# Performance work log

Hardware: AMD Instinct MI355X
Metric: run time of the kernel (lower is better)

Reference implementation:

```python
import jax, jax.numpy as jnp
import numpy as np

B, D, T = 32, 256, 2048
Z_NUM, Z_DIM = 1024, 256


def setup_inputs() -> dict:
    key = jax.random.key(0)
    k1, k2 = jax.random.split(key)
    z = jax.random.normal(k1, (B, D, T), dtype=jnp.float32)
    embedding = jax.random.normal(k2, (Z_NUM, Z_DIM), dtype=jnp.float32)
    return {"z": z, "embedding": embedding}


def reference(z, embedding):
    # z: [B, D, T] (time_last=True), embedding: [z_num, z_dim]
    Bv, Dv, Tv = z.shape
    sg = jax.lax.stop_gradient
    # flatten to [N, D] with N = B*T
    zf = jnp.transpose(z, (0, 2, 1)).reshape(-1, Dv)
    # squared-euclidean distances [N, z_num]
    distances = (jnp.sum(zf * zf, axis=1, keepdims=True)
                 + jnp.sum(embedding * embedding, axis=1)
                 - 2.0 * (zf @ embedding.T))
    encoding_idx = jnp.argmin(distances, axis=1)          # [N]
    z_vq = embedding[encoding_idx]                        # [N, D] codebook gather
    # perplexity via scatter-add histogram (equiv. to one-hot scatter + column sum)
    counts = jnp.zeros((embedding.shape[0],), zf.dtype).at[encoding_idx].add(1.0)
    avg_probs = counts / zf.shape[0]
    perplexity = jnp.exp(-jnp.sum(avg_probs * jnp.log(avg_probs + 1e-10)))
    # commitment / codebook losses (reduction='mean', normalize=False)
    z_qut_loss = jnp.mean((z_vq - sg(zf)) ** 2)
    z_enc_loss = jnp.mean((sg(z_vq) - zf) ** 2)
    # straight-through estimator
    z_vq_st = zf + sg(z_vq - zf)
    out = jnp.transpose(z_vq_st.reshape(Bv, Tv, Dv), (0, 2, 1))  # back to [B, D, T]
    return out, z_qut_loss, z_enc_loss, perplexity
```

## Files before the change

### kernel.cpp

```cpp
#include <hip/hip_runtime.h>


typedef _Float16 f16;
typedef _Float16 f16x8 __attribute__((ext_vector_type(8)));
typedef float f32x4 __attribute__((ext_vector_type(4)));

#define NROWS 65536
#define THRESH 0.02f
#define AMB_CAP 32768

#define MERGE_T2(v1, i1, v2, i2, ov1, oi1, ov2, oi2)                      \
  do {                                                                    \
    if (ov1 < v1 || (ov1 == v1 && oi1 < i1)) {                            \
      if (v1 < ov2 || (v1 == ov2 && i1 < oi2)) { v2 = v1; i2 = i1; }      \
      else { v2 = ov2; i2 = oi2; }                                        \
      v1 = ov1; i1 = oi1;                                                 \
    } else if (ov1 < v2 || (ov1 == v2 && oi1 < i2)) { v2 = ov1; i2 = oi1; } \
  } while (0)

__global__ void k0_prep(const float* __restrict__ emb, f16* __restrict__ eh,
                        f16* __restrict__ el, float* __restrict__ enorm,
                        float* __restrict__ counts, float* __restrict__ loss,
                        int* __restrict__ ambc) {
  int c = blockIdx.x, d = threadIdx.x;
  float v = emb[c * 256 + d];
  f16 h = (f16)v;
  f16 l = (f16)(v - (float)h);
  eh[c * 256 + d] = h;
  el[c * 256 + d] = l;
  float s = v * v;
#pragma unroll
  for (int o = 32; o; o >>= 1) s += __shfl_down(s, o, 64);
  __shared__ float red[4];
  if ((d & 63) == 0) red[d >> 6] = s;
  __syncthreads();
  if (d == 0) enorm[c] = red[0] + red[1] + red[2] + red[3];
  if (c == 0) {
    for (int i = d; i < 1024; i += 256) counts[i] = 0.f;
    if (d == 0) { *loss = 0.f; *ambc = 0; }
  }
}

__global__ void kp_split(const float* __restrict__ z, f16* __restrict__ zh,
                         f16* __restrict__ zl) {
  __shared__ float F[64][65];
  int bid = blockIdx.x;
  int b = bid >> 7;
  int rem = bid & 127;
  int t0 = (rem >> 2) << 6;
  int dd0 = (rem & 3) << 6;
  int tid = threadIdx.x;
  int tl = tid & 63, dr = tid >> 6;
  const float* zp = z + ((size_t)b * 256 + dd0 + dr) * 2048 + t0 + tl;
#pragma unroll
  for (int i = 0; i < 16; ++i)
    F[dr + i * 4][tl] = zp[(size_t)i * 4 * 2048];
  __syncthreads();
  int r = tid >> 2, q = tid & 3;
  f16x8 h0, h1, l0, l1;
#pragma unroll
  for (int j = 0; j < 8; ++j) {
    float v = F[q * 16 + j][r];
    f16 h = (f16)v; h0[j] = h; l0[j] = (f16)(v - (float)h);
  }
#pragma unroll
  for (int j = 0; j < 8; ++j) {
    float v = F[q * 16 + 8 + j][r];
    f16 h = (f16)v; h1[j] = h; l1[j] = (f16)(v - (float)h);
  }
  size_t n = (size_t)b * 2048 + t0 + r;
  f16* ph = zh + n * 256 + dd0 + q * 16;
  f16* pl = zl + n * 256 + dd0 + q * 16;
  *(f16x8*)(ph) = h0; *(f16x8*)(ph + 8) = h1;
  *(f16x8*)(pl) = l0; *(f16x8*)(pl + 8) = l1;
}

__device__ __forceinline__ void k1_epilogue(
    f32x4 (&acc)[4][4], const float* en_s, float* rv1, int* ri1, float* rv2, int* ri2,
    int tid, int wr, int wc, int g, int r16, int rowTile, int chunk, int cBase,
    float* cv1, int* ci1, float* cv2, int* ci2) {
  float en[4];
#pragma unroll
  for (int ni = 0; ni < 4; ++ni) en[ni] = en_s[wc * 64 + ni * 16 + r16];
#pragma unroll
  for (int mi = 0; mi < 4; ++mi) {
#pragma unroll
    for (int r = 0; r < 4; ++r) {
      float v1 = 1e38f, v2 = 1e38f; int i1 = 0x7fffffff, i2 = 0x7fffffff;
#pragma unroll
      for (int ni = 0; ni < 4; ++ni) {
        float v = en[ni] - 2.0f * acc[mi][ni][r];
        int idx = cBase + wc * 64 + ni * 16 + r16;
        if (v < v1 || (v == v1 && idx < i1)) { v2 = v1; i2 = i1; v1 = v; i1 = idx; }
        else if (v < v2 || (v == v2 && idx < i2)) { v2 = v; i2 = idx; }
      }
#pragma unroll
      for (int o = 1; o < 16; o <<= 1) {
        float ov1 = __shfl_xor(v1, o, 64); int oi1 = __shfl_xor(i1, o, 64);
        float ov2 = __shfl_xor(v2, o, 64); int oi2 = __shfl_xor(i2, o, 64);
        MERGE_T2(v1, i1, v2, i2, ov1, oi1, ov2, oi2);
      }
      if (r16 == 0) {
        int row = wr * 64 + mi * 16 + g * 4 + r;
        rv1[row * 2 + wc] = v1; ri1[row * 2 + wc] = i1;
        rv2[row * 2 + wc] = v2; ri2[row * 2 + wc] = i2;
      }
    }
  }
  __syncthreads();
  if (tid < 128) {
    float v1 = rv1[tid * 2], ov1 = rv1[tid * 2 + 1];
    int   i1 = ri1[tid * 2], oi1 = ri1[tid * 2 + 1];
    float v2 = rv2[tid * 2], ov2 = rv2[tid * 2 + 1];
    int   i2 = ri2[tid * 2], oi2 = ri2[tid * 2 + 1];
    MERGE_T2(v1, i1, v2, i2, ov1, oi1, ov2, oi2);
    size_t n = (size_t)rowTile * 128 + tid;
    cv1[(size_t)chunk * NROWS + n] = v1;
    ci1[(size_t)chunk * NROWS + n] = i1;
    cv2[(size_t)chunk * NROWS + n] = v2;
    ci2[(size_t)chunk * NROWS + n] = i2;
  }
}

__launch_bounds__(256, 2)
__global__ void k1p_argmin(const f16* __restrict__ zh, const f16* __restrict__ zl,
                           const f16* __restrict__ eh, const f16* __restrict__ el,
                           const float* __restrict__ enorm,
                           float* __restrict__ cv1, int* __restrict__ ci1,
                           float* __restrict__ cv2, int* __restrict__ ci2) {
  __shared__ f16x8 Ah[128 * 5], Al[128 * 5], Bh[128 * 5], Bl[128 * 5];
  __shared__ float en_s[128];
  __shared__ float rv1[256], rv2[256];
  __shared__ int ri1[256], ri2[256];

  int bid = blockIdx.x;
  int x = bid & 7, j = bid >> 3;
  int rowTile = x * 64 + (j >> 3);
  int chunk = j & 7;
  int n0 = rowTile * 128;
  int cBase = chunk << 7;

  int tid = threadIdx.x;
  int lane = tid & 63;
  int wid = tid >> 6;
  int wr = wid >> 1, wc = wid & 1;
  int g = lane >> 4, r16 = lane & 15;

  if (tid < 128) en_s[tid] = enorm[cBase + tid];

  f32x4 acc[4][4] = {};

  int tt = tid & 127;
  int kk2 = tid >> 7;
  const f16* zhb = zh + ((size_t)(n0 + tt)) * 256 + kk2 * 16;
  const f16* zlb = zl + ((size_t)(n0 + tt)) * 256 + kk2 * 16;
  const f16* ehb = eh + ((size_t)(cBase + tt)) * 256 + kk2 * 16;
  const f16* elb = el + ((size_t)(cBase + tt)) * 256 + kk2 * 16;
  int s0 = tt * 5 + kk2 * 2, s1 = s0 + 1;

  for (int ks = 0; ks < 8; ++ks) {
    if (ks) __syncthreads();
    Ah[s0] = *(const f16x8*)(zhb + ks * 32);
    Ah[s1] = *(const f16x8*)(zhb + ks * 32 + 8);
    Al[s0] = *(const f16x8*)(zlb + ks * 32);
    Al[s1] = *(const f16x8*)(zlb + ks * 32 + 8);
    Bh[s0] = *(const f16x8*)(ehb + ks * 32);
    Bh[s1] = *(const f16x8*)(ehb + ks * 32 + 8);
    Bl[s0] = *(const f16x8*)(elb + ks * 32);
    Bl[s1] = *(const f16x8*)(elb + ks * 32 + 8);
    __syncthreads();
    f16x8 ah[4], al[4], bh[4], bl[4];
#pragma unroll
    for (int mi = 0; mi < 4; ++mi) {
      int row = wr * 64 + mi * 16 + r16;
      ah[mi] = Ah[row * 5 + g];
      al[mi] = Al[row * 5 + g];
    }
#pragma unroll
    for (int ni = 0; ni < 4; ++ni) {
      int code = wc * 64 + ni * 16 + r16;
      bh[ni] = Bh[code * 5 + g];
      bl[ni] = Bl[code * 5 + g];
    }
#pragma unroll
    for (int mi = 0; mi < 4; ++mi)
#pragma unroll
      for (int ni = 0; ni < 4; ++ni) {
        acc[mi][ni] = __builtin_amdgcn_mfma_f32_16x16x32_f16(ah[mi], bh[ni], acc[mi][ni], 0, 0, 0);
        acc[mi][ni] = __builtin_amdgcn_mfma_f32_16x16x32_f16(ah[mi], bl[ni], acc[mi][ni], 0, 0, 0);
        acc[mi][ni] = __builtin_amdgcn_mfma_f32_16x16x32_f16(al[mi], bh[ni], acc[mi][ni], 0, 0, 0);
      }
  }
  k1_epilogue(acc, en_s, rv1, ri1, rv2, ri2, tid, wr, wc, g, r16, rowTile, chunk,
              cBase, cv1, ci1, cv2, ci2);
}

__launch_bounds__(256, 2)
__global__ void k1_argmin(const float* __restrict__ z, const f16* __restrict__ eh,
                          const f16* __restrict__ el, const float* __restrict__ enorm,
                          float* __restrict__ cv1, int* __restrict__ ci1,
                          float* __restrict__ cv2, int* __restrict__ ci2) {
  __shared__ f16x8 Ah[128 * 5], Al[128 * 5], Bh[128 * 5], Bl[128 * 5];
  __shared__ float en_s[128];
  __shared__ float rv1[256], rv2[256];
  __shared__ int ri1[256], ri2[256];

  int bid = blockIdx.x;
  int x = bid & 7, j = bid >> 3;
  int rowTile = x * 64 + (j >> 3);
  int chunk = j & 7;
  int bb = rowTile >> 4;
  int t0 = (rowTile & 15) << 7;
  int cBase = chunk << 7;

  int tid = threadIdx.x;
  int lane = tid & 63;
  int wid = tid >> 6;
  int wr = wid >> 1, wc = wid & 1;
  int g = lane >> 4, r16 = lane & 15;

  if (tid < 128) en_s[tid] = enorm[cBase + tid];

  f32x4 acc[4][4] = {};

  int tt = tid & 127;
  int kk2 = tid >> 7;
  const float* zbase = z + ((size_t)bb * 256 + kk2 * 16) * 2048 + t0 + tt;
  const f16* ehbase = eh + ((size_t)(cBase + tt)) * 256 + kk2 * 16;
  const f16* elbase = el + ((size_t)(cBase + tt)) * 256 + kk2 * 16;
  int s0 = tt * 5 + kk2 * 2, s1 = s0 + 1;

  for (int ks = 0; ks < 8; ++ks) {
    if (ks) __syncthreads();
    {
      const float* zp = zbase + (size_t)ks * 32 * 2048;
      f16x8 h8, l8;
#pragma unroll
      for (int cj = 0; cj < 8; ++cj) {
        float v = zp[cj * 2048];
        f16 h = (f16)v; h8[cj] = h; l8[cj] = (f16)(v - (float)h);
      }
      Ah[s0] = h8; Al[s0] = l8;
#pragma unroll
      for (int cj = 0; cj < 8; ++cj) {
        float v = zp[(8 + cj) * 2048];
        f16 h = (f16)v; h8[cj] = h; l8[cj] = (f16)(v - (float)h);
      }
      Ah[s1] = h8; Al[s1] = l8;
    }
    {
      const f16* ep = ehbase + ks * 32;
      Bh[s0] = *(const f16x8*)(ep);
      Bh[s1] = *(const f16x8*)(ep + 8);
      const f16* ep2 = elbase + ks * 32;
      Bl[s0] = *(const f16x8*)(ep2);
      Bl[s1] = *(const f16x8*)(ep2 + 8);
    }
    __syncthreads();
    f16x8 ah[4], al[4], bh[4], bl[4];
#pragma unroll
    for (int mi = 0; mi < 4; ++mi) {
      int row = wr * 64 + mi * 16 + r16;
      ah[mi] = Ah[row * 5 + g];
      al[mi] = Al[row * 5 + g];
    }
#pragma unroll
    for (int ni = 0; ni < 4; ++ni) {
      int code = wc * 64 + ni * 16 + r16;
      bh[ni] = Bh[code * 5 + g];
      bl[ni] = Bl[code * 5 + g];
    }
#pragma unroll
    for (int mi = 0; mi < 4; ++mi)
#pragma unroll
      for (int ni = 0; ni < 4; ++ni) {
        acc[mi][ni] = __builtin_amdgcn_mfma_f32_16x16x32_f16(ah[mi], bh[ni], acc[mi][ni], 0, 0, 0);
        acc[mi][ni] = __builtin_amdgcn_mfma_f32_16x16x32_f16(ah[mi], bl[ni], acc[mi][ni], 0, 0, 0);
        acc[mi][ni] = __builtin_amdgcn_mfma_f32_16x16x32_f16(al[mi], bh[ni], acc[mi][ni], 0, 0, 0);
      }
  }
  k1_epilogue(acc, en_s, rv1, ri1, rv2, ri2, tid, wr, wc, g, r16, rowTile, chunk,
              cBase, cv1, ci1, cv2, ci2);
}

__global__ void k2_select(const float* __restrict__ cv1, const int* __restrict__ ci1,
                          const float* __restrict__ cv2, const int* __restrict__ ci2,
                          int* __restrict__ fidx, int* __restrict__ ambc,
                          int* __restrict__ amb_list) {
  int n = blockIdx.x * 256 + threadIdx.x;
  float g1 = 1e38f, g2 = 1e38f; int gi1 = 0x7fffffff, gi2 = 0x7fffffff;
#pragma unroll
  for (int c = 0; c < 8; ++c) {
    float ov1 = cv1[c * NROWS + n]; int oi1 = ci1[c * NROWS + n];
    float ov2 = cv2[c * NROWS + n]; int oi2 = ci2[c * NROWS + n];
    MERGE_T2(g1, gi1, g2, gi2, ov1, oi1, ov2, oi2);
  }
  fidx[n] = gi1;
  if (g2 - g1 < THRESH) {
    int pos = atomicAdd(ambc, 1);
    if (pos < AMB_CAP) amb_list[pos] = n;
  }
}

__global__ void k2b_rescore(const float* __restrict__ z, const float* __restrict__ emb,
                            const float* __restrict__ enorm,
                            const int* __restrict__ ci1, const int* __restrict__ ci2,
                            const int* __restrict__ ambc, const int* __restrict__ amb_list,
                            int* __restrict__ fidx) {
  int cnt = *ambc; if (cnt > AMB_CAP) cnt = AMB_CAP;
  int lane = threadIdx.x & 63;
  int wglobal = (blockIdx.x * 256 + threadIdx.x) >> 6;
  for (int a = wglobal; a < cnt; a += 256) {
    int n = amb_list[a];
    int bb = n >> 11, t = n & 2047;
    float zr[4];
#pragma unroll
    for (int jj = 0; jj < 4; ++jj)
      zr[jj] = z[((size_t)bb * 256 + lane * 4 + jj) * 2048 + t];
    float zn = zr[0] * zr[0] + zr[1] * zr[1] + zr[2] * zr[2] + zr[3] * zr[3];
#pragma unroll
    for (int o = 1; o < 64; o <<= 1) zn += __shfl_xor(zn, o, 64);
    float bv = 1e38f; int bi = 0x7fffffff;
    for (int cc = 0; cc < 16; ++cc) {
      int c = cc >> 1;
      int cand = (cc & 1) ? ci2[c * NROWS + n] : ci1[c * NROWS + n];
      const float4* e4p = (const float4*)(emb + (size_t)cand * 256);
      float4 e4 = e4p[lane];
      float s = zr[0] * e4.x + zr[1] * e4.y + zr[2] * e4.z + zr[3] * e4.w;
#pragma unroll
      for (int o = 1; o < 64; o <<= 1) s += __shfl_xor(s, o, 64);
      float d = zn + enorm[cand] - 2.0f * s;
      if (d < bv || (d == bv && cand < bi)) { bv = d; bi = cand; }
    }
    if (lane == 0) fidx[n] = bi;
  }
}

__global__ void k3_gather(const float* __restrict__ z, const float* __restrict__ emb,
                          const int* __restrict__ fidx, float* __restrict__ out,
                          float* __restrict__ counts, float* __restrict__ loss) {
  __shared__ int sidx[128];
  __shared__ float red[4];
  int rowTile = blockIdx.x;
  int bb = rowTile >> 4;
  int t0 = (rowTile & 15) << 7;
  int tid = threadIdx.x;
  if (tid < 128) sidx[tid] = fidx[rowTile * 128 + tid];
  __syncthreads();
  int q = tid & 31, dh = (tid >> 5) << 5;
  const float* e0 = emb + (size_t)sidx[q * 4 + 0] * 256;
  const float* e1 = emb + (size_t)sidx[q * 4 + 1] * 256;
  const float* e2 = emb + (size_t)sidx[q * 4 + 2] * 256;
  const float* e3 = emb + (size_t)sidx[q * 4 + 3] * 256;
  size_t zb = ((size_t)bb * 256 + dh) * 2048 + t0 + q * 4;
  float ls = 0.f;
  for (int i = 0; i < 32; ++i) {
    int d = dh + i;
    float4 z4 = *(const float4*)(z + zb + (size_t)i * 2048);
    float4 e4 = make_float4(e0[d], e1[d], e2[d], e3[d]);
    *(float4*)(out + zb + (size_t)i * 2048) = e4;
    float da = e4.x - z4.x, db = e4.y - z4.y, dc = e4.z - z4.z, dd = e4.w - z4.w;
    ls += da * da + db * db + dc * dc + dd * dd;
  }
#pragma unroll
  for (int o = 32; o; o >>= 1) ls += __shfl_down(ls, o, 64);
  if ((tid & 63) == 0) red[tid >> 6] = ls;
  __syncthreads();
  if (tid == 0) atomicAdd(loss, red[0] + red[1] + red[2] + red[3]);
  if (tid < 128) atomicAdd(counts + sidx[tid], 1.0f);
}

__global__ void k4_final(const float* __restrict__ counts, const float* __restrict__ loss,
                         float* __restrict__ outs) {
  __shared__ float red[4];
  int tid = threadIdx.x;
  float h = 0.f;
  for (int i = tid; i < 1024; i += 256) {
    float p = counts[i] * (1.0f / 65536.0f);
    h += p * logf(p + 1e-10f);
  }
#pragma unroll
  for (int o = 32; o; o >>= 1) h += __shfl_down(h, o, 64);
  if ((tid & 63) == 0) red[tid >> 6] = h;
  __syncthreads();
  if (tid == 0) {
    float H = red[0] + red[1] + red[2] + red[3];
    float perp = expf(-H);
    float l = *loss * (1.0f / 16777216.0f);
    outs[0] = l;
    outs[1] = l;
    outs[2] = perp;
  }
}

extern "C" void kernel_launch(void* const* d_in, const int* in_sizes, int n_in,
                              void* d_out, int out_size, void* d_ws, size_t ws_size,
                              hipStream_t stream) {
  const float* z = (const float*)d_in[0];
  const float* emb = (const float*)d_in[1];
  float* out = (float*)d_out;
  char* ws = (char*)d_ws;
  f16*   eh     = (f16*)(ws);
  f16*   el     = (f16*)(ws + (512u << 10));
  float* enorm  = (float*)(ws + (1u << 20));
  float* counts = (float*)(ws + (1u << 20) + 4096);
  float* lossp  = (float*)(ws + (1u << 20) + 8192);
  int*   ambc   = (int*)  (ws + (1u << 20) + 8196);
  int*   amb_l  = (int*)  (ws + (1u << 20) + 16384);
  float* cv1    = (float*)(ws + (2u << 20));
  int*   ci1    = (int*)  (ws + (4u << 20));
  float* cv2    = (float*)(ws + (6u << 20));
  int*   ci2    = (int*)  (ws + (8u << 20));
  int*   fidx   = (int*)  (ws + (10u << 20));
  f16*   zh     = (f16*)(ws + (11u << 20));
  f16*   zl     = (f16*)(ws + (43u << 20));
  const size_t NEED_PRESPLIT = 75u << 20;

  hipLaunchKernelGGL(k0_prep, dim3(1024), dim3(256), 0, stream, emb, eh, el, enorm, counts, lossp, ambc);
  if (ws_size >= NEED_PRESPLIT) {
    hipLaunchKernelGGL(kp_split,   dim3(4096), dim3(256), 0, stream, z, zh, zl);
    hipLaunchKernelGGL(k1p_argmin, dim3(4096), dim3(256), 0, stream, zh, zl, eh, el, enorm, cv1, ci1, cv2, ci2);
  } else {
    hipLaunchKernelGGL(k1_argmin,  dim3(4096), dim3(256), 0, stream, z, eh, el, enorm, cv1, ci1, cv2, ci2);
  }
  hipLaunchKernelGGL(k2_select,   dim3(256), dim3(256), 0, stream, cv1, ci1, cv2, ci2, fidx, ambc, amb_l);
  hipLaunchKernelGGL(k2b_rescore, dim3(64),  dim3(256), 0, stream, z, emb, enorm, ci1, ci2, ambc, amb_l, fidx);
  hipLaunchKernelGGL(k3_gather,   dim3(512), dim3(256), 0, stream, z, emb, fidx, out, counts, lossp);
  hipLaunchKernelGGL(k4_final,    dim3(1),   dim3(256), 0, stream, counts, lossp, out + 16777216);
}
```

Before: 396.2 us.

## Pre-tile split operands and stage them with direct global-to-LDS loads

The split-precision z and codebook halves are now written in a tile-blocked layout matching the MFMA fragment order, so each k-step's tile is one contiguous block. The argmin kernel then fills shared memory with global_load_lds 16-byte transfers instead of going through registers. It reads fragments without padding, and occupancy is raised to 3 blocks per CU. The fallback path that split z on the fly is removed, so the kernel now always assumes a large enough workspace. The unpadded layout may cause LDS bank conflicts, and the direct-to-LDS transfers still wait on full barriers.

```diff
diff --git a/kernel.cpp b/kernel.cpp
--- a/kernel.cpp
+++ b/kernel.cpp
@@ -18,6 +18,12 @@
     } else if (ov1 < v2 || (ov1 == v2 && oi1 < i2)) { v2 = ov1; i2 = oi1; } \
   } while (0)
 
+__device__ __forceinline__ void gl16(const void* g, void* l) {
+  __builtin_amdgcn_global_load_lds(
+      (const __attribute__((address_space(1))) unsigned int*)g,
+      (__attribute__((address_space(3))) unsigned int*)l, 16, 0, 0);
+}
+
 __global__ void k0_prep(const float* __restrict__ emb, f16* __restrict__ eh,
                         f16* __restrict__ el, float* __restrict__ enorm,
                         float* __restrict__ counts, float* __restrict__ loss,
@@ -26,8 +32,11 @@
   float v = emb[c * 256 + d];
   f16 h = (f16)v;
   f16 l = (f16)(v - (float)h);
-  eh[c * 256 + d] = h;
-  el[c * 256 + d] = l;
+  int chunk = c >> 7, crow = c & 127;
+  int ks = d >> 5, gg = (d >> 3) & 3, e = d & 7;
+  size_t off = ((((size_t)chunk * 8 + ks) * 4 + gg) * 128 + crow) * 8 + e;
+  eh[off] = h;
+  el[off] = l;
   float s = v * v;
 #pragma unroll
   for (int o = 32; o; o >>= 1) s += __shfl_down(s, o, 64);
@@ -68,17 +77,79 @@
     float v = F[q * 16 + 8 + j][r];
     f16 h = (f16)v; h1[j] = h; l1[j] = (f16)(v - (float)h);
   }
-  size_t n = (size_t)b * 2048 + t0 + r;
-  f16* ph = zh + n * 256 + dd0 + q * 16;
-  f16* pl = zl + n * 256 + dd0 + q * 16;
-  *(f16x8*)(ph) = h0; *(f16x8*)(ph + 8) = h1;
-  *(f16x8*)(pl) = l0; *(f16x8*)(pl + 8) = l1;
-}
-
-__device__ __forceinline__ void k1_epilogue(
-    f32x4 (&acc)[4][4], const float* en_s, float* rv1, int* ri1, float* rv2, int* ri2,
-    int tid, int wr, int wc, int g, int r16, int rowTile, int chunk, int cBase,
-    float* cv1, int* ci1, float* cv2, int* ci2) {
+  int n = b * 2048 + t0 + r;
+  int rt = n >> 7, row = n & 127;
+  int d0 = dd0 + q * 16;
+  int ks = d0 >> 5, g0 = (d0 >> 3) & 3;
+  size_t base = ((((size_t)rt * 8 + ks) * 4 + g0) * 128 + row) * 8;
+  *(f16x8*)(zh + base) = h0; *(f16x8*)(zh + base + 1024) = h1;
+  *(f16x8*)(zl + base) = l0; *(f16x8*)(zl + base + 1024) = l1;
+}
+
+__launch_bounds__(256, 3)
+__global__ void k1p_argmin(const f16* __restrict__ zh, const f16* __restrict__ zl,
+                           const f16* __restrict__ eh, const f16* __restrict__ el,
+                           const float* __restrict__ enorm,
+                           float* __restrict__ cv1, int* __restrict__ ci1,
+                           float* __restrict__ cv2, int* __restrict__ ci2) {
+  __shared__ f16x8 Ah[512], Al[512], Bh[512], Bl[512];
+  __shared__ float en_s[128];
+  __shared__ float rv1[256], rv2[256];
+  __shared__ int ri1[256], ri2[256];
+
+  int bid = blockIdx.x;
+  int x = bid & 7, j = bid >> 3;
+  int rowTile = x * 64 + (j >> 3);
+  int chunk = j & 7;
+  int cBase = chunk << 7;
+
+  int tid = threadIdx.x;
+  int lane = tid & 63;
+  int w = tid >> 6;
+  int wr = w >> 1, wc = w & 1;
+  int g = lane >> 4, r16 = lane & 15;
+
+  if (tid < 128) en_s[tid] = enorm[cBase + tid];
+
+  f32x4 acc[4][4] = {};
+
+  const char* gAh = (const char*)zh + (size_t)rowTile * 65536 + w * 2048 + lane * 16;
+  const char* gAl = (const char*)zl + (size_t)rowTile * 65536 + w * 2048 + lane * 16;
+  const char* gBh = (const char*)eh + (size_t)chunk * 65536 + w * 2048 + lane * 16;
+  const char* gBl = (const char*)el + (size_t)chunk * 65536 + w * 2048 + lane * 16;
+  char* lAh = (char*)Ah + w * 2048;
+  char* lAl = (char*)Al + w * 2048;
+  char* lBh = (char*)Bh + w * 2048;
+  char* lBl = (char*)Bl + w * 2048;
+
+  for (int ks = 0; ks < 8; ++ks) {
+    if (ks) __syncthreads();
+    size_t go = (size_t)ks * 8192;
+    gl16(gAh + go, lAh);  gl16(gAh + go + 1024, lAh + 1024);
+    gl16(gAl + go, lAl);  gl16(gAl + go + 1024, lAl + 1024);
+    gl16(gBh + go, lBh);  gl16(gBh + go + 1024, lBh + 1024);
+    gl16(gBl + go, lBl);  gl16(gBl + go + 1024, lBl + 1024);
+    __syncthreads();
+    f16x8 bh[4], bl[4];
+#pragma unroll
+    for (int ni = 0; ni < 4; ++ni) {
+      int code = wc * 64 + ni * 16 + r16;
+      bh[ni] = Bh[g * 128 + code];
+      bl[ni] = Bl[g * 128 + code];
+    }
+#pragma unroll
+    for (int mi = 0; mi < 4; ++mi) {
+      int row = wr * 64 + mi * 16 + r16;
+      f16x8 ah = Ah[g * 128 + row];
+      f16x8 al = Al[g * 128 + row];
+#pragma unroll
+      for (int ni = 0; ni < 4; ++ni) {
+        acc[mi][ni] = __builtin_amdgcn_mfma_f32_16x16x32_f16(ah, bh[ni], acc[mi][ni], 0, 0, 0);
+        acc[mi][ni] = __builtin_amdgcn_mfma_f32_16x16x32_f16(ah, bl[ni], acc[mi][ni], 0, 0, 0);
+        acc[mi][ni] = __builtin_amdgcn_mfma_f32_16x16x32_f16(al, bh[ni], acc[mi][ni], 0, 0, 0);
+      }
+    }
+  }
   float en[4];
 #pragma unroll
   for (int ni = 0; ni < 4; ++ni) en[ni] = en_s[wc * 64 + ni * 16 + r16];
@@ -120,167 +191,6 @@
     cv2[(size_t)chunk * NROWS + n] = v2;
     ci2[(size_t)chunk * NROWS + n] = i2;
   }
-}
-
-__launch_bounds__(256, 2)
-__global__ void k1p_argmin(const f16* __restrict__ zh, const f16* __restrict__ zl,
-                           const f16* __restrict__ eh, const f16* __restrict__ el,
-                           const float* __restrict__ enorm,
-                           float* __restrict__ cv1, int* __restrict__ ci1,
-                           float* __restrict__ cv2, int* __restrict__ ci2) {
-  __shared__ f16x8 Ah[128 * 5], Al[128 * 5], Bh[128 * 5], Bl[128 * 5];
-  __shared__ float en_s[128];
-  __shared__ float rv1[256], rv2[256];
-  __shared__ int ri1[256], ri2[256];
-
-  int bid = blockIdx.x;
-  int x = bid & 7, j = bid >> 3;
-  int rowTile = x * 64 + (j >> 3);
-  int chunk = j & 7;
-  int n0 = rowTile * 128;
-  int cBase = chunk << 7;
-
-  int tid = threadIdx.x;
-  int lane = tid & 63;
-  int wid = tid >> 6;
-  int wr = wid >> 1, wc = wid & 1;
-  int g = lane >> 4, r16 = lane & 15;
-
-  if (tid < 128) en_s[tid] = enorm[cBase + tid];
-
-  f32x4 acc[4][4] = {};
-
-  int tt = tid & 127;
-  int kk2 = tid >> 7;
-  const f16* zhb = zh + ((size_t)(n0 + tt)) * 256 + kk2 * 16;
-  const f16* zlb = zl + ((size_t)(n0 + tt)) * 256 + kk2 * 16;
-  const f16* ehb = eh + ((size_t)(cBase + tt)) * 256 + kk2 * 16;
-  const f16* elb = el + ((size_t)(cBase + tt)) * 256 + kk2 * 16;
-  int s0 = tt * 5 + kk2 * 2, s1 = s0 + 1;
-
-  for (int ks = 0; ks < 8; ++ks) {
-    if (ks) __syncthreads();
-    Ah[s0] = *(const f16x8*)(zhb + ks * 32);
-    Ah[s1] = *(const f16x8*)(zhb + ks * 32 + 8);
-    Al[s0] = *(const f16x8*)(zlb + ks * 32);
-    Al[s1] = *(const f16x8*)(zlb + ks * 32 + 8);
-    Bh[s0] = *(const f16x8*)(ehb + ks * 32);
-    Bh[s1] = *(const f16x8*)(ehb + ks * 32 + 8);
-    Bl[s0] = *(const f16x8*)(elb + ks * 32);
-    Bl[s1] = *(const f16x8*)(elb + ks * 32 + 8);
-    __syncthreads();
-    f16x8 ah[4], al[4], bh[4], bl[4];
-#pragma unroll
-    for (int mi = 0; mi < 4; ++mi) {
-      int row = wr * 64 + mi * 16 + r16;
-      ah[mi] = Ah[row * 5 + g];
-      al[mi] = Al[row * 5 + g];
-    }
-#pragma unroll
-    for (int ni = 0; ni < 4; ++ni) {
-      int code = wc * 64 + ni * 16 + r16;
-      bh[ni] = Bh[code * 5 + g];
-      bl[ni] = Bl[code * 5 + g];
-    }
-#pragma unroll
-    for (int mi = 0; mi < 4; ++mi)
-#pragma unroll
-      for (int ni = 0; ni < 4; ++ni) {
-        acc[mi][ni] = __builtin_amdgcn_mfma_f32_16x16x32_f16(ah[mi], bh[ni], acc[mi][ni], 0, 0, 0);
-        acc[mi][ni] = __builtin_amdgcn_mfma_f32_16x16x32_f16(ah[mi], bl[ni], acc[mi][ni], 0, 0, 0);
-        acc[mi][ni] = __builtin_amdgcn_mfma_f32_16x16x32_f16(al[mi], bh[ni], acc[mi][ni], 0, 0, 0);
-      }
-  }
-  k1_epilogue(acc, en_s, rv1, ri1, rv2, ri2, tid, wr, wc, g, r16, rowTile, chunk,
-              cBase, cv1, ci1, cv2, ci2);
-}
-
-__launch_bounds__(256, 2)
-__global__ void k1_argmin(const float* __restrict__ z, const f16* __restrict__ eh,
-                          const f16* __restrict__ el, const float* __restrict__ enorm,
-                          float* __restrict__ cv1, int* __restrict__ ci1,
-                          float* __restrict__ cv2, int* __restrict__ ci2) {
-  __shared__ f16x8 Ah[128 * 5], Al[128 * 5], Bh[128 * 5], Bl[128 * 5];
-  __shared__ float en_s[128];
-  __shared__ float rv1[256], rv2[256];
-  __shared__ int ri1[256], ri2[256];
-
-  int bid = blockIdx.x;
-  int x = bid & 7, j = bid >> 3;
-  int rowTile = x * 64 + (j >> 3);
-  int chunk = j & 7;
-  int bb = rowTile >> 4;
-  int t0 = (rowTile & 15) << 7;
-  int cBase = chunk << 7;
-
-  int tid = threadIdx.x;
-  int lane = tid & 63;
-  int wid = tid >> 6;
-  int wr = wid >> 1, wc = wid & 1;
-  int g = lane >> 4, r16 = lane & 15;
-
-  if (tid < 128) en_s[tid] = enorm[cBase + tid];
-
-  f32x4 acc[4][4] = {};
-
-  int tt = tid & 127;
-  int kk2 = tid >> 7;
-  const float* zbase = z + ((size_t)bb * 256 + kk2 * 16) * 2048 + t0 + tt;
-  const f16* ehbase = eh + ((size_t)(cBase + tt)) * 256 + kk2 * 16;
-  const f16* elbase = el + ((size_t)(cBase + tt)) * 256 + kk2 * 16;
-  int s0 = tt * 5 + kk2 * 2, s1 = s0 + 1;
-
-  for (int ks = 0; ks < 8; ++ks) {
-    if (ks) __syncthreads();
-    {
-      const float* zp = zbase + (size_t)ks * 32 * 2048;
-      f16x8 h8, l8;
-#pragma unroll
-      for (int cj = 0; cj < 8; ++cj) {
-        float v = zp[cj * 2048];
-        f16 h = (f16)v; h8[cj] = h; l8[cj] = (f16)(v - (float)h);
-      }
-      Ah[s0] = h8; Al[s0] = l8;
-#pragma unroll
-      for (int cj = 0; cj < 8; ++cj) {
-        float v = zp[(8 + cj) * 2048];
-        f16 h = (f16)v; h8[cj] = h; l8[cj] = (f16)(v - (float)h);
-      }
-      Ah[s1] = h8; Al[s1] = l8;
-    }
-    {
-      const f16* ep = ehbase + ks * 32;
-      Bh[s0] = *(const f16x8*)(ep);
-      Bh[s1] = *(const f16x8*)(ep + 8);
-      const f16* ep2 = elbase + ks * 32;
-      Bl[s0] = *(const f16x8*)(ep2);
-      Bl[s1] = *(const f16x8*)(ep2 + 8);
-    }
-    __syncthreads();
-    f16x8 ah[4], al[4], bh[4], bl[4];
-#pragma unroll
-    for (int mi = 0; mi < 4; ++mi) {
-      int row = wr * 64 + mi * 16 + r16;
-      ah[mi] = Ah[row * 5 + g];
-      al[mi] = Al[row * 5 + g];
-    }
-#pragma unroll
-    for (int ni = 0; ni < 4; ++ni) {
-      int code = wc * 64 + ni * 16 + r16;
-      bh[ni] = Bh[code * 5 + g];
-      bl[ni] = Bl[code * 5 + g];
-    }
-#pragma unroll
-    for (int mi = 0; mi < 4; ++mi)
-#pragma unroll
-      for (int ni = 0; ni < 4; ++ni) {
-        acc[mi][ni] = __builtin_amdgcn_mfma_f32_16x16x32_f16(ah[mi], bh[ni], acc[mi][ni], 0, 0, 0);
-        acc[mi][ni] = __builtin_amdgcn_mfma_f32_16x16x32_f16(ah[mi], bl[ni], acc[mi][ni], 0, 0, 0);
-        acc[mi][ni] = __builtin_amdgcn_mfma_f32_16x16x32_f16(al[mi], bh[ni], acc[mi][ni], 0, 0, 0);
-      }
-  }
-  k1_epilogue(acc, en_s, rv1, ri1, rv2, ri2, tid, wr, wc, g, r16, rowTile, chunk,
-              cBase, cv1, ci1, cv2, ci2);
 }
 
 __global__ void k2_select(const float* __restrict__ cv1, const int* __restrict__ ci1,
@@ -414,15 +324,10 @@
   int*   fidx   = (int*)  (ws + (10u << 20));
   f16*   zh     = (f16*)(ws + (11u << 20));
   f16*   zl     = (f16*)(ws + (43u << 20));
-  const size_t NEED_PRESPLIT = 75u << 20;
-
-  hipLaunchKernelGGL(k0_prep, dim3(1024), dim3(256), 0, stream, emb, eh, el, enorm, counts, lossp, ambc);
-  if (ws_size >= NEED_PRESPLIT) {
-    hipLaunchKernelGGL(kp_split,   dim3(4096), dim3(256), 0, stream, z, zh, zl);
-    hipLaunchKernelGGL(k1p_argmin, dim3(4096), dim3(256), 0, stream, zh, zl, eh, el, enorm, cv1, ci1, cv2, ci2);
-  } else {
-    hipLaunchKernelGGL(k1_argmin,  dim3(4096), dim3(256), 0, stream, z, eh, el, enorm, cv1, ci1, cv2, ci2);
-  }
+
+  hipLaunchKernelGGL(k0_prep,     dim3(1024), dim3(256), 0, stream, emb, eh, el, enorm, counts, lossp, ambc);
+  hipLaunchKernelGGL(kp_split,    dim3(4096), dim3(256), 0, stream, z, zh, zl);
+  hipLaunchKernelGGL(k1p_argmin,  dim3(4096), dim3(256), 0, stream, zh, zl, eh, el, enorm, cv1, ci1, cv2, ci2);
   hipLaunchKernelGGL(k2_select,   dim3(256), dim3(256), 0, stream, cv1, ci1, cv2, ci2, fidx, ambc, amb_l);
   hipLaunchKernelGGL(k2b_rescore, dim3(64),  dim3(256), 0, stream, z, emb, enorm, ci1, ci2, ambc, amb_l, fidx);
   hipLaunchKernelGGL(k3_gather,   dim3(512), dim3(256), 0, stream, z, emb, fidx, out, counts, lossp);
```

After: 360.3 us. 9.1% less time.
